# Performance work log

Measured on AMD Instinct MI355X. Metric: run time of the kernel, lower is better.

The kernel has to match this reference:

```python
import jax, jax.numpy as jnp
import numpy as np

N = 50000
E = 800000
IN_CH = 128
HID = 32
HEADS = 4
OUT_CH = 40
LEAKY = 0.2
BN_EPS = 1e-5


def _gat_layer(x, src, dst, W, a_src, a_dst, b, n_nodes, concat):
    # x: [N, F_in], W: [F_in, H*C], a_src/a_dst: [H, C], b: [H*C] or [C]
    H, C = a_src.shape
    h = (x @ W).reshape(n_nodes, H, C)                      # [N, H, C]
    e_s = jnp.einsum('nhc,hc->nh', h, a_src)                # [N, H]
    e_d = jnp.einsum('nhc,hc->nh', h, a_dst)                # [N, H]
    e = e_s[src] + e_d[dst]                                 # [E, H]
    e = jnp.where(e > 0, e, LEAKY * e)                      # LeakyReLU
    # segment softmax over incoming edges of each destination node
    m = jax.ops.segment_max(e, dst, num_segments=n_nodes)   # [N, H]
    ex = jnp.exp(e - m[dst])
    s = jax.ops.segment_sum(ex, dst, num_segments=n_nodes)  # [N, H]
    alpha = ex / s[dst]                                     # [E, H]
    out = jax.ops.segment_sum(h[src] * alpha[:, :, None], dst,
                              num_segments=n_nodes)         # [N, H, C]
    out = out.reshape(n_nodes, H * C) if concat else out.mean(axis=1)
    return out + b


def setup_inputs() -> dict:
    key = jax.random.key(0)
    ks = jax.random.split(key, 16)
    d1 = HEADS * HID  # 128
    inp = {
        'x': jax.random.normal(ks[0], (N, IN_CH), dtype=jnp.float32),
        'edge_index': jax.random.randint(ks[1], (2, E), 0, N, dtype=jnp.int64),
        # conv1 params (heads=4, concat)
        'W1': jax.random.normal(ks[2], (IN_CH, d1), dtype=jnp.float32) * 0.1,
        'a1_src': jax.random.normal(ks[3], (HEADS, HID), dtype=jnp.float32) * 0.1,
        'a1_dst': jax.random.normal(ks[4], (HEADS, HID), dtype=jnp.float32) * 0.1,
        'b1': jnp.zeros((d1,), dtype=jnp.float32),
        # BatchNorm1d(128) in eval mode
        'bn_gamma': jnp.ones((d1,), dtype=jnp.float32),
        'bn_beta': jnp.zeros((d1,), dtype=jnp.float32),
        'bn_mean': jax.random.normal(ks[5], (d1,), dtype=jnp.float32) * 0.1,
        'bn_var': jax.random.uniform(ks[6], (d1,), minval=0.5, maxval=1.5, dtype=jnp.float32),
        # conv2 params (heads=1, concat=False)
        'W2': jax.random.normal(ks[7], (d1, OUT_CH), dtype=jnp.float32) * 0.1,
        'a2_src': jax.random.normal(ks[8], (1, OUT_CH), dtype=jnp.float32) * 0.1,
        'a2_dst': jax.random.normal(ks[9], (1, OUT_CH), dtype=jnp.float32) * 0.1,
        'b2': jnp.zeros((OUT_CH,), dtype=jnp.float32),
    }
    return inp


def reference(x, edge_index, W1, a1_src, a1_dst, b1, bn_gamma, bn_beta,
              bn_mean, bn_var, W2, a2_src, a2_dst, b2):
    n = x.shape[0]
    loops = jnp.arange(n, dtype=edge_index.dtype)
    src = jnp.concatenate([edge_index[0], loops])  # PyG GATConv adds self-loops
    dst = jnp.concatenate([edge_index[1], loops])
    h = _gat_layer(x, src, dst, W1, a1_src, a1_dst, b1, n, concat=True)
    h = (h - bn_mean) / jnp.sqrt(bn_var + BN_EPS) * bn_gamma + bn_beta  # BN eval
    h = jax.nn.elu(h)
    # dropout is identity in eval mode
    out = _gat_layer(h, src, dst, W2, a2_src, a2_dst, b2, n, concat=False)
    return jax.nn.log_softmax(out, axis=1)
```

## Files before the change

kernel.cpp:

```cpp
#include <hip/hip_runtime.h>
#include <hip/hip_bf16.h>
#include <math.h>

#define NN 50000
#define NE 800000
#define ETOT (NE + NN)
#define LEAKY 0.2f
#define BN_EPS 1e-5f

#define NB 256
#define BSZ 196
#define NBB 128
#define EPB ((ETOT + NBB - 1) / NBB)

#define BN1 144
#define BN2 48

typedef unsigned short u16;
typedef unsigned int u32;
typedef short s16;
typedef __attribute__((ext_vector_type(8))) short bf16x8;
typedef __attribute__((ext_vector_type(4))) float f32x4;

__device__ __forceinline__ float bf2f(u32 u) {
    union { u32 i; float f; } x; x.i = u << 16; return x.f;
}
__device__ __forceinline__ u16 f2bf(float f) {
    __hip_bfloat16 b = __float2bfloat16(f);
    return *reinterpret_cast<u16*>(&b);
}


__global__ __launch_bounds__(256) void k_binA(const int* __restrict__ ei,
                                              int* __restrict__ cnt) {
    __shared__ int hist[NB];
    int t = threadIdx.x;
    for (int i = t; i < NB; i += 256) hist[i] = 0;
    __syncthreads();
    int e0 = blockIdx.x * EPB, e1 = min(e0 + EPB, ETOT);
    for (int e = e0 + t; e < e1; e += 256) {
        int dst = (e < NE) ? ei[NE + e] : (e - NE);
        atomicAdd(&hist[dst / BSZ], 1);
    }
    __syncthreads();
    for (int b = t; b < NB; b += 256) cnt[b * NBB + blockIdx.x] = hist[b];
}

__global__ __launch_bounds__(256) void k_scanA(const int* __restrict__ in,
                                               int* __restrict__ out,
                                               int* __restrict__ bsums, int n) {
    __shared__ int sh[256];
    int t = threadIdx.x;
    int i = blockIdx.x * 256 + t;
    int v = (i < n) ? in[i] : 0;
    sh[t] = v;
    __syncthreads();
    #pragma unroll
    for (int off = 1; off < 256; off <<= 1) {
        int u = (t >= off) ? sh[t - off] : 0;
        __syncthreads();
        sh[t] += u;
        __syncthreads();
    }
    if (i < n) out[i] = sh[t] - v;
    if (t == 255) bsums[blockIdx.x] = sh[t];
}

__global__ __launch_bounds__(256) void k_scanB(int* __restrict__ bsums, int nb) {
    __shared__ int sh[256];
    int t = threadIdx.x;
    int v = (t < nb) ? bsums[t] : 0;
    sh[t] = v;
    __syncthreads();
    #pragma unroll
    for (int off = 1; off < 256; off <<= 1) {
        int u = (t >= off) ? sh[t - off] : 0;
        __syncthreads();
        sh[t] += u;
        __syncthreads();
    }
    if (t < nb) bsums[t] = sh[t] - v;
}

__global__ void k_scanC(int* __restrict__ out, const int* __restrict__ bsums, int n) {
    int i = blockIdx.x * blockDim.x + threadIdx.x;
    if (i < n) out[i] += bsums[i >> 8];
}

__global__ __launch_bounds__(256) void k_binB(const int* __restrict__ ei,
                                              const int* __restrict__ excl,
                                              u32* __restrict__ packed) {
    __shared__ int cur[NB];
    int t = threadIdx.x;
    for (int b = t; b < NB; b += 256) cur[b] = excl[b * NBB + blockIdx.x];
    __syncthreads();
    int e0 = blockIdx.x * EPB, e1 = min(e0 + EPB, ETOT);
    for (int e = e0 + t; e < e1; e += 256) {
        int src, dst;
        if (e < NE) { src = ei[e]; dst = ei[NE + e]; }
        else        { src = e - NE; dst = e - NE; }
        int pos = atomicAdd(&cur[dst / BSZ], 1);
        packed[pos] = ((u32)src << 16) | (u32)dst;
    }
}

__global__ __launch_bounds__(256) void k_binC(const u32* __restrict__ packed,
                                              const int* __restrict__ excl,
                                              int* __restrict__ offsets,
                                              int* __restrict__ ssrc) {
    __shared__ int hist[256];
    __shared__ int sc[256];
    __shared__ int cur[256];
    int b = blockIdx.x, t = threadIdx.x;
    int n0 = b * BSZ;
    int base = excl[b * NBB];
    int next = (b < NB - 1) ? excl[(b + 1) * NBB] : ETOT;
    int total = next - base;
    hist[t] = 0;
    __syncthreads();
    for (int i = t; i < total; i += 256) {
        int dst = (int)(packed[base + i] & 0xffffu);
        atomicAdd(&hist[dst - n0], 1);
    }
    __syncthreads();
    int v = hist[t];
    sc[t] = v;
    __syncthreads();
    #pragma unroll
    for (int off = 1; off < 256; off <<= 1) {
        int u = (t >= off) ? sc[t - off] : 0;
        __syncthreads();
        sc[t] += u;
        __syncthreads();
    }
    int exl = sc[t] - v;
    int node = n0 + t;
    if (t <= BSZ && node <= NN) {
        if (t < BSZ || node == NN) offsets[node] = base + exl;
    }
    cur[t] = exl;
    __syncthreads();
    for (int i = t; i < total; i += 256) {
        u32 pv = packed[base + i];
        int dst = (int)(pv & 0xffffu);
        int pos = atomicAdd(&cur[dst - n0], 1);
        ssrc[base + pos] = (int)(pv >> 16);
    }
}

__global__ void k_prep(const float* __restrict__ W1, const float* __restrict__ a1s,
                       const float* __restrict__ a1d, const float* __restrict__ W2,
                       const float* __restrict__ a2s, const float* __restrict__ a2d,
                       u16* __restrict__ Wt1, u16* __restrict__ Wt2) {
    int tid = blockIdx.x * blockDim.x + threadIdx.x;
    int nth = gridDim.x * blockDim.x;
    for (int idx = tid; idx < BN1 * 128; idx += nth) {
        int n = idx >> 7, k = idx & 127;
        float v = 0.f;
        if (n < 128) v = W1[k * 128 + n];
        else if (n < 132) {
            int h = n - 128; float s = 0.f;
            for (int c = 0; c < 32; ++c) s += W1[k * 128 + h * 32 + c] * a1s[h * 32 + c];
            v = s;
        } else if (n < 136) {
            int h = n - 132; float s = 0.f;
            for (int c = 0; c < 32; ++c) s += W1[k * 128 + h * 32 + c] * a1d[h * 32 + c];
            v = s;
        }
        Wt1[idx] = f2bf(v);
    }
    for (int idx = tid; idx < BN2 * 128; idx += nth) {
        int n = idx >> 7, k = idx & 127;
        float v = 0.f;
        if (n < 40) v = W2[k * 40 + n];
        else if (n == 40) { float s = 0.f; for (int c = 0; c < 40; ++c) s += W2[k * 40 + c] * a2s[c]; v = s; }
        else if (n == 41) { float s = 0.f; for (int c = 0; c < 40; ++c) s += W2[k * 40 + c] * a2d[c]; v = s; }
        Wt2[idx] = f2bf(v);
    }
}

__global__ __launch_bounds__(256) void k_mm1(const float* __restrict__ x,
                                             const u16* __restrict__ Wt1,
                                             u16* __restrict__ h1b,
                                             float* __restrict__ es1,
                                             float* __restrict__ ed1) {
    __shared__ __align__(16) s16 As[128 * 128];
    __shared__ __align__(16) s16 Bs[BN1 * 128];
    int t = threadIdx.x;
    int row0 = blockIdx.x * 128;
    #pragma unroll
    for (int i = 0; i < 16; ++i) {
        int c = t + i * 256;
        int r = c >> 5, k0 = (c & 31) * 4;
        float4 v = make_float4(0.f, 0.f, 0.f, 0.f);
        int row = row0 + r;
        if (row < NN) v = *(const float4*)&x[(size_t)row * 128 + k0];
        u16 pk[4] = {f2bf(v.x), f2bf(v.y), f2bf(v.z), f2bf(v.w)};
        int byte = (r * 256 + k0 * 2) ^ ((r & 7) << 4);
        *(uint2*)((char*)As + byte) = *(uint2*)pk;
    }
    #pragma unroll
    for (int i = 0; i < 9; ++i) {
        int c = t + i * 256;
        int n = c >> 4, k0 = (c & 15) * 8;
        uint4 v = *(const uint4*)&Wt1[n * 128 + k0];
        int byte = (n * 256 + k0 * 2) ^ ((n & 7) << 4);
        *(uint4*)((char*)Bs + byte) = v;
    }
    __syncthreads();
    int wave = t >> 6, lane = t & 63;
    int lr = lane & 15, lq = lane >> 4;
    int wrow = wave * 32;
    f32x4 acc[2][9];
    #pragma unroll
    for (int a = 0; a < 2; ++a)
        #pragma unroll
        for (int b = 0; b < 9; ++b) acc[a][b] = (f32x4){0.f, 0.f, 0.f, 0.f};
    #pragma unroll
    for (int ks = 0; ks < 4; ++ks) {
        int kb = ks * 32 + lq * 8;
        bf16x8 af[2];
        #pragma unroll
        for (int rb = 0; rb < 2; ++rb) {
            int r = wrow + rb * 16 + lr;
            int byte = (r * 256 + kb * 2) ^ ((r & 7) << 4);
            af[rb] = *(bf16x8*)((char*)As + byte);
        }
        #pragma unroll
        for (int cb = 0; cb < 9; ++cb) {
            int n = cb * 16 + lr;
            int byte = (n * 256 + kb * 2) ^ ((n & 7) << 4);
            bf16x8 bfr = *(bf16x8*)((char*)Bs + byte);
            acc[0][cb] = __builtin_amdgcn_mfma_f32_16x16x32_bf16(af[0], bfr, acc[0][cb], 0, 0, 0);
            acc[1][cb] = __builtin_amdgcn_mfma_f32_16x16x32_bf16(af[1], bfr, acc[1][cb], 0, 0, 0);
        }
    }
    #pragma unroll
    for (int rb = 0; rb < 2; ++rb) {
        #pragma unroll
        for (int cb = 0; cb < 9; ++cb) {
            #pragma unroll
            for (int r = 0; r < 4; ++r) {
                int row = row0 + wrow + rb * 16 + lq * 4 + r;
                int col = cb * 16 + lr;
                if (row < NN) {
                    float v = acc[rb][cb][r];
                    if (col < 128) h1b[(size_t)row * 128 + col] = f2bf(v);
                    else if (col < 132) es1[row * 4 + (col - 128)] = v;
                    else if (col < 136) ed1[row * 4 + (col - 132)] = v;
                }
            }
        }
    }
}

__global__ __launch_bounds__(256) void k_mm2(const u16* __restrict__ hbnb,
                                             const u16* __restrict__ Wt2,
                                             float* __restrict__ h2,
                                             float* __restrict__ es2,
                                             float* __restrict__ ed2) {
    __shared__ __align__(16) s16 As[128 * 128];
    __shared__ __align__(16) s16 Bs[BN2 * 128];
    int t = threadIdx.x;
    int row0 = blockIdx.x * 128;
    #pragma unroll
    for (int i = 0; i < 8; ++i) {
        int c = t + i * 256;
        int r = c >> 4, k0 = (c & 15) * 8;
        uint4 v = make_uint4(0, 0, 0, 0);
        int row = row0 + r;
        if (row < NN) v = *(const uint4*)&hbnb[(size_t)row * 128 + k0];
        int byte = (r * 256 + k0 * 2) ^ ((r & 7) << 4);
        *(uint4*)((char*)As + byte) = v;
    }
    #pragma unroll
    for (int i = 0; i < 3; ++i) {
        int c = t + i * 256;
        int n = c >> 4, k0 = (c & 15) * 8;
        uint4 v = *(const uint4*)&Wt2[n * 128 + k0];
        int byte = (n * 256 + k0 * 2) ^ ((n & 7) << 4);
        *(uint4*)((char*)Bs + byte) = v;
    }
    __syncthreads();
    int wave = t >> 6, lane = t & 63;
    int lr = lane & 15, lq = lane >> 4;
    int wrow = wave * 32;
    f32x4 acc[2][3];
    #pragma unroll
    for (int a = 0; a < 2; ++a)
        #pragma unroll
        for (int b = 0; b < 3; ++b) acc[a][b] = (f32x4){0.f, 0.f, 0.f, 0.f};
    #pragma unroll
    for (int ks = 0; ks < 4; ++ks) {
        int kb = ks * 32 + lq * 8;
        bf16x8 af[2];
        #pragma unroll
        for (int rb = 0; rb < 2; ++rb) {
            int r = wrow + rb * 16 + lr;
            int byte = (r * 256 + kb * 2) ^ ((r & 7) << 4);
            af[rb] = *(bf16x8*)((char*)As + byte);
        }
        #pragma unroll
        for (int cb = 0; cb < 3; ++cb) {
            int n = cb * 16 + lr;
            int byte = (n * 256 + kb * 2) ^ ((n & 7) << 4);
            bf16x8 bfr = *(bf16x8*)((char*)Bs + byte);
            acc[0][cb] = __builtin_amdgcn_mfma_f32_16x16x32_bf16(af[0], bfr, acc[0][cb], 0, 0, 0);
            acc[1][cb] = __builtin_amdgcn_mfma_f32_16x16x32_bf16(af[1], bfr, acc[1][cb], 0, 0, 0);
        }
    }
    #pragma unroll
    for (int rb = 0; rb < 2; ++rb) {
        #pragma unroll
        for (int cb = 0; cb < 3; ++cb) {
            #pragma unroll
            for (int r = 0; r < 4; ++r) {
                int row = row0 + wrow + rb * 16 + lq * 4 + r;
                int col = cb * 16 + lr;
                if (row < NN) {
                    float v = acc[rb][cb][r];
                    if (col < 40) h2[(size_t)row * 40 + col] = v;
                    else if (col == 40) es2[row] = v;
                    else if (col == 41) ed2[row] = v;
                }
            }
        }
    }
}

__global__ __launch_bounds__(256) void k_agg1(
        const u16* __restrict__ h1b, const float* __restrict__ es,
        const float* __restrict__ ed, const int* __restrict__ offsets,
        const int* __restrict__ ssrc, const float* __restrict__ b1,
        const float* __restrict__ gamma, const float* __restrict__ beta,
        const float* __restrict__ mean, const float* __restrict__ var,
        u16* __restrict__ hbnb) {
    __shared__ float wlds[4][64][4];
    int wv = threadIdx.x >> 6;
    int node = blockIdx.x * 4 + wv;
    if (node >= NN) return;
    int l = threadIdx.x & 63;
    int head = l >> 4;
    int p0 = offsets[node], p1 = offsets[node + 1];
    float4 ed4 = *(const float4*)&ed[(size_t)node * 4];
    float4 sw4 = make_float4(0.f, 0.f, 0.f, 0.f);
    float acc0 = 0.f, acc1 = 0.f;
    const float* wp = &wlds[wv][0][head];
    for (int base = p0; base < p1; base += 64) {
        int cnt = min(64, p1 - base);
        int myidx = (l < cnt) ? ssrc[base + l] : 0;
        float4 w4 = make_float4(0.f, 0.f, 0.f, 0.f);
        if (l < cnt) {
            float4 e4 = *(const float4*)&es[(size_t)myidx * 4];
            float tv;
            tv = e4.x + ed4.x; tv = tv > 0.f ? tv : LEAKY * tv; w4.x = __expf(tv);
            tv = e4.y + ed4.y; tv = tv > 0.f ? tv : LEAKY * tv; w4.y = __expf(tv);
            tv = e4.z + ed4.z; tv = tv > 0.f ? tv : LEAKY * tv; w4.z = __expf(tv);
            tv = e4.w + ed4.w; tv = tv > 0.f ? tv : LEAKY * tv; w4.w = __expf(tv);
        }
        *(float4*)&wlds[wv][l][0] = w4;
        sw4.x += w4.x; sw4.y += w4.y; sw4.z += w4.z; sw4.w += w4.w;
        int j = 0;
        for (; j + 8 <= cnt; j += 8) {
            int s0 = __shfl(myidx, j);
            int s1 = __shfl(myidx, j + 1);
            int s2 = __shfl(myidx, j + 2);
            int s3 = __shfl(myidx, j + 3);
            int s4 = __shfl(myidx, j + 4);
            int s5 = __shfl(myidx, j + 5);
            int s6 = __shfl(myidx, j + 6);
            int s7 = __shfl(myidx, j + 7);
            u32 w0 = *(const u32*)&h1b[(size_t)s0 * 128 + 2 * l];
            u32 w1 = *(const u32*)&h1b[(size_t)s1 * 128 + 2 * l];
            u32 w2 = *(const u32*)&h1b[(size_t)s2 * 128 + 2 * l];
            u32 w3 = *(const u32*)&h1b[(size_t)s3 * 128 + 2 * l];
            u32 w4g = *(const u32*)&h1b[(size_t)s4 * 128 + 2 * l];
            u32 w5 = *(const u32*)&h1b[(size_t)s5 * 128 + 2 * l];
            u32 w6 = *(const u32*)&h1b[(size_t)s6 * 128 + 2 * l];
            u32 w7 = *(const u32*)&h1b[(size_t)s7 * 128 + 2 * l];
            float x0 = wp[(j + 0) * 4];
            float x1 = wp[(j + 1) * 4];
            float x2 = wp[(j + 2) * 4];
            float x3 = wp[(j + 3) * 4];
            float x4 = wp[(j + 4) * 4];
            float x5 = wp[(j + 5) * 4];
            float x6 = wp[(j + 6) * 4];
            float x7 = wp[(j + 7) * 4];
            acc0 = fmaf(x0, bf2f(w0 & 0xffffu), acc0);
            acc1 = fmaf(x0, bf2f(w0 >> 16), acc1);
            acc0 = fmaf(x1, bf2f(w1 & 0xffffu), acc0);
            acc1 = fmaf(x1, bf2f(w1 >> 16), acc1);
            acc0 = fmaf(x2, bf2f(w2 & 0xffffu), acc0);
            acc1 = fmaf(x2, bf2f(w2 >> 16), acc1);
            acc0 = fmaf(x3, bf2f(w3 & 0xffffu), acc0);
            acc1 = fmaf(x3, bf2f(w3 >> 16), acc1);
            acc0 = fmaf(x4, bf2f(w4g & 0xffffu), acc0);
            acc1 = fmaf(x4, bf2f(w4g >> 16), acc1);
            acc0 = fmaf(x5, bf2f(w5 & 0xffffu), acc0);
            acc1 = fmaf(x5, bf2f(w5 >> 16), acc1);
            acc0 = fmaf(x6, bf2f(w6 & 0xffffu), acc0);
            acc1 = fmaf(x6, bf2f(w6 >> 16), acc1);
            acc0 = fmaf(x7, bf2f(w7 & 0xffffu), acc0);
            acc1 = fmaf(x7, bf2f(w7 >> 16), acc1);
        }
        for (; j + 4 <= cnt; j += 4) {
            int s0 = __shfl(myidx, j);
            int s1 = __shfl(myidx, j + 1);
            int s2 = __shfl(myidx, j + 2);
            int s3 = __shfl(myidx, j + 3);
            u32 w0 = *(const u32*)&h1b[(size_t)s0 * 128 + 2 * l];
            u32 w1 = *(const u32*)&h1b[(size_t)s1 * 128 + 2 * l];
            u32 w2 = *(const u32*)&h1b[(size_t)s2 * 128 + 2 * l];
            u32 w3 = *(const u32*)&h1b[(size_t)s3 * 128 + 2 * l];
            float x0 = wp[(j + 0) * 4];
            float x1 = wp[(j + 1) * 4];
            float x2 = wp[(j + 2) * 4];
            float x3 = wp[(j + 3) * 4];
            acc0 = fmaf(x0, bf2f(w0 & 0xffffu), acc0);
            acc1 = fmaf(x0, bf2f(w0 >> 16), acc1);
            acc0 = fmaf(x1, bf2f(w1 & 0xffffu), acc0);
            acc1 = fmaf(x1, bf2f(w1 >> 16), acc1);
            acc0 = fmaf(x2, bf2f(w2 & 0xffffu), acc0);
            acc1 = fmaf(x2, bf2f(w2 >> 16), acc1);
            acc0 = fmaf(x3, bf2f(w3 & 0xffffu), acc0);
            acc1 = fmaf(x3, bf2f(w3 >> 16), acc1);
        }
        for (; j < cnt; ++j) {
            int s0 = __shfl(myidx, j);
            u32 w0 = *(const u32*)&h1b[(size_t)s0 * 128 + 2 * l];
            float x0 = wp[j * 4];
            acc0 = fmaf(x0, bf2f(w0 & 0xffffu), acc0);
            acc1 = fmaf(x0, bf2f(w0 >> 16), acc1);
        }
    }
    #pragma unroll
    for (int off = 1; off < 64; off <<= 1) {
        sw4.x += __shfl_xor(sw4.x, off);
        sw4.y += __shfl_xor(sw4.y, off);
        sw4.z += __shfl_xor(sw4.z, off);
        sw4.w += __shfl_xor(sw4.w, off);
    }
    float s = (head == 0) ? sw4.x : (head == 1) ? sw4.y : (head == 2) ? sw4.z : sw4.w;
    float inv = 1.f / s;
    int i0 = 2 * l, i1 = 2 * l + 1;
    float o0 = acc0 * inv + b1[i0];
    float o1 = acc1 * inv + b1[i1];
    o0 = (o0 - mean[i0]) * rsqrtf(var[i0] + BN_EPS) * gamma[i0] + beta[i0];
    o1 = (o1 - mean[i1]) * rsqrtf(var[i1] + BN_EPS) * gamma[i1] + beta[i1];
    o0 = o0 > 0.f ? o0 : __expf(o0) - 1.f;
    o1 = o1 > 0.f ? o1 : __expf(o1) - 1.f;
    u32 pk = (u32)f2bf(o0) | ((u32)f2bf(o1) << 16);
    *(u32*)&hbnb[(size_t)node * 128 + 2 * l] = pk;
}

__global__ __launch_bounds__(256) void k_agg2(
        const float* __restrict__ h2, const float* __restrict__ es,
        const float* __restrict__ ed, const int* __restrict__ offsets,
        const int* __restrict__ ssrc, const float* __restrict__ b2,
        float* __restrict__ out) {
    int node = blockIdx.x * 4 + (threadIdx.x >> 6);
    if (node >= NN) return;
    int l = threadIdx.x & 63;
    int lmod = (l < 40) ? l : (l - 40);
    int p0 = offsets[node], p1 = offsets[node + 1];
    float edv = ed[node];
    float swacc = 0.f, acc = 0.f;
    bool pay = (l < 40);
    for (int base = p0; base < p1; base += 64) {
        int cnt = min(64, p1 - base);
        int myidx = (l < cnt) ? ssrc[base + l] : 0;
        float mw = 0.f;
        if (l < cnt) {
            float e = es[myidx] + edv;
            e = e > 0.f ? e : LEAKY * e;
            mw = __expf(e);
        }
        swacc += mw;
        int j = 0;
        for (; j + 8 <= cnt; j += 8) {
            int s0 = __shfl(myidx, j);
            int s1 = __shfl(myidx, j + 1);
            int s2 = __shfl(myidx, j + 2);
            int s3 = __shfl(myidx, j + 3);
            int s4 = __shfl(myidx, j + 4);
            int s5 = __shfl(myidx, j + 5);
            int s6 = __shfl(myidx, j + 6);
            int s7 = __shfl(myidx, j + 7);
            float x0 = __shfl(mw, j);
            float x1 = __shfl(mw, j + 1);
            float x2 = __shfl(mw, j + 2);
            float x3 = __shfl(mw, j + 3);
            float x4 = __shfl(mw, j + 4);
            float x5 = __shfl(mw, j + 5);
            float x6 = __shfl(mw, j + 6);
            float x7 = __shfl(mw, j + 7);
            float h0 = h2[(size_t)s0 * 40 + lmod];
            float h1v = h2[(size_t)s1 * 40 + lmod];
            float h2v = h2[(size_t)s2 * 40 + lmod];
            float h3 = h2[(size_t)s3 * 40 + lmod];
            float h4 = h2[(size_t)s4 * 40 + lmod];
            float h5 = h2[(size_t)s5 * 40 + lmod];
            float h6 = h2[(size_t)s6 * 40 + lmod];
            float h7 = h2[(size_t)s7 * 40 + lmod];
            acc = fmaf(x0, h0, acc);
            acc = fmaf(x1, h1v, acc);
            acc = fmaf(x2, h2v, acc);
            acc = fmaf(x3, h3, acc);
            acc = fmaf(x4, h4, acc);
            acc = fmaf(x5, h5, acc);
            acc = fmaf(x6, h6, acc);
            acc = fmaf(x7, h7, acc);
        }
        for (; j + 4 <= cnt; j += 4) {
            int s0 = __shfl(myidx, j);
            int s1 = __shfl(myidx, j + 1);
            int s2 = __shfl(myidx, j + 2);
            int s3 = __shfl(myidx, j + 3);
            float x0 = __shfl(mw, j);
            float x1 = __shfl(mw, j + 1);
            float x2 = __shfl(mw, j + 2);
            float x3 = __shfl(mw, j + 3);
            float h0 = h2[(size_t)s0 * 40 + lmod];
            float h1v = h2[(size_t)s1 * 40 + lmod];
            float h2v = h2[(size_t)s2 * 40 + lmod];
            float h3 = h2[(size_t)s3 * 40 + lmod];
            acc = fmaf(x0, h0, acc);
            acc = fmaf(x1, h1v, acc);
            acc = fmaf(x2, h2v, acc);
            acc = fmaf(x3, h3, acc);
        }
        for (; j < cnt; ++j) {
            int s0 = __shfl(myidx, j);
            float x0 = __shfl(mw, j);
            float h0 = h2[(size_t)s0 * 40 + lmod];
            acc = fmaf(x0, h0, acc);
        }
    }
    float s = swacc;
    #pragma unroll
    for (int off = 1; off < 64; off <<= 1) s += __shfl_xor(s, off);
    float v = acc / s + (pay ? b2[l] : 0.f);
    float mv = pay ? v : -1e30f;
    #pragma unroll
    for (int off = 1; off < 64; off <<= 1) mv = fmaxf(mv, __shfl_xor(mv, off));
    float ex = pay ? __expf(v - mv) : 0.f;
    #pragma unroll
    for (int off = 1; off < 64; off <<= 1) ex += __shfl_xor(ex, off);
    if (pay) out[(size_t)node * 40 + l] = v - mv - __logf(ex);
}

extern "C" void kernel_launch(void* const* d_in, const int* in_sizes, int n_in,
                              void* d_out, int out_size, void* d_ws, size_t ws_size,
                              hipStream_t stream) {
    const float* x   = (const float*)d_in[0];
    const int*   ei  = (const int*)d_in[1];
    const float* W1  = (const float*)d_in[2];
    const float* a1s = (const float*)d_in[3];
    const float* a1d = (const float*)d_in[4];
    const float* b1  = (const float*)d_in[5];
    const float* bng = (const float*)d_in[6];
    const float* bnb = (const float*)d_in[7];
    const float* bnm = (const float*)d_in[8];
    const float* bnv = (const float*)d_in[9];
    const float* W2  = (const float*)d_in[10];
    const float* a2s = (const float*)d_in[11];
    const float* a2d = (const float*)d_in[12];
    const float* b2  = (const float*)d_in[13];
    float* out = (float*)d_out;

    char* ws = (char*)d_ws;
    size_t off = 0;
    auto alloc = [&](size_t bytes) -> void* {
        void* p = ws + off;
        off = (off + bytes + 255) & ~(size_t)255;
        return p;
    };
    int*   cntb     = (int*)alloc((size_t)NB * NBB * 4);
    int*   excl     = (int*)alloc((size_t)NB * NBB * 4);
    int*   bsums    = (int*)alloc((size_t)NBB * 4);
    int*   offsets  = (int*)alloc((size_t)(NN + 1) * 4);
    u32*   packed   = (u32*)alloc((size_t)ETOT * 4);
    int*   ssrc     = (int*)alloc((size_t)ETOT * 4);
    u16*   Wt1      = (u16*)alloc((size_t)BN1 * 128 * 2);
    u16*   Wt2      = (u16*)alloc((size_t)BN2 * 128 * 2);
    u16*   h1b      = (u16*)alloc((size_t)NN * 128 * 2);
    float* es1      = (float*)alloc((size_t)NN * 4 * 4);
    float* ed1      = (float*)alloc((size_t)NN * 4 * 4);
    u16*   hbnb     = (u16*)alloc((size_t)NN * 128 * 2);
    float* h2       = (float*)alloc((size_t)NN * 40 * 4);
    float* es2      = (float*)alloc((size_t)NN * 4);
    float* ed2      = (float*)alloc((size_t)NN * 4);

    const int nscan = NB * NBB;
    k_prep<<<80, 256, 0, stream>>>(W1, a1s, a1d, W2, a2s, a2d, Wt1, Wt2);
    k_binA<<<NBB, 256, 0, stream>>>(ei, cntb);
    k_scanA<<<nscan / 256, 256, 0, stream>>>(cntb, excl, bsums, nscan);
    k_scanB<<<1, 256, 0, stream>>>(bsums, NBB);
    k_scanC<<<nscan / 256, 256, 0, stream>>>(excl, bsums, nscan);
    k_binB<<<NBB, 256, 0, stream>>>(ei, excl, packed);
    k_binC<<<NB, 256, 0, stream>>>(packed, excl, offsets, ssrc);
    k_mm1<<<(NN + 127) / 128, 256, 0, stream>>>(x, Wt1, h1b, es1, ed1);
    k_agg1<<<(NN + 3) / 4, 256, 0, stream>>>(h1b, es1, ed1, offsets, ssrc,
                                             b1, bng, bnb, bnm, bnv, hbnb);
    k_mm2<<<(NN + 127) / 128, 256, 0, stream>>>(hbnb, Wt2, h2, es2, ed2);
    k_agg2<<<(NN + 3) / 4, 256, 0, stream>>>(h2, es2, ed2, offsets, ssrc, b2, out);
}
```

Before: 146.7 us.

## Gather layer-1 neighbor rows with 16-byte loads across four edge groups

The layer-1 aggregation now splits each wave into four 16-lane groups, each handling a different edge. Each lane loads 8 bf16 channels with one 16-byte load instead of a 4-byte load per edge per lane, and the four partial sums are merged with cross-lane shuffles at the end. The aim is to cut the number of gather load instructions and make each edge's 256-byte row a single wide access. In exchange it adds more accumulator registers, clamped or masked tail iterations, and a final reduction, and only a quarter of the lanes do the epilogue.

```diff
diff --git a/kernel.cpp b/kernel.cpp
--- a/kernel.cpp
+++ b/kernel.cpp
@@ -24,6 +24,12 @@
 
 __device__ __forceinline__ float bf2f(u32 u) {
     union { u32 i; float f; } x; x.i = u << 16; return x.f;
+}
+__device__ __forceinline__ float bf2f_lo(u32 u) {
+    union { u32 i; float f; } x; x.i = u << 16; return x.f;
+}
+__device__ __forceinline__ float bf2f_hi(u32 u) {
+    union { u32 i; float f; } x; x.i = u & 0xffff0000u; return x.f;
 }
 __device__ __forceinline__ u16 f2bf(float f) {
     __hip_bfloat16 b = __float2bfloat16(f);
@@ -340,12 +346,15 @@
     int node = blockIdx.x * 4 + wv;
     if (node >= NN) return;
     int l = threadIdx.x & 63;
-    int head = l >> 4;
+    int g = l >> 4;
+    int c16 = l & 15;
+    int h = c16 >> 2;
     int p0 = offsets[node], p1 = offsets[node + 1];
     float4 ed4 = *(const float4*)&ed[(size_t)node * 4];
     float4 sw4 = make_float4(0.f, 0.f, 0.f, 0.f);
-    float acc0 = 0.f, acc1 = 0.f;
-    const float* wp = &wlds[wv][0][head];
+    float acc[8];
+    #pragma unroll
+    for (int i = 0; i < 8; ++i) acc[i] = 0.f;
     for (int base = p0; base < p1; base += 64) {
         int cnt = min(64, p1 - base);
         int myidx = (l < cnt) ? ssrc[base + l] : 0;
@@ -360,78 +369,38 @@
         }
         *(float4*)&wlds[wv][l][0] = w4;
         sw4.x += w4.x; sw4.y += w4.y; sw4.z += w4.z; sw4.w += w4.w;
-        int j = 0;
-        for (; j + 8 <= cnt; j += 8) {
-            int s0 = __shfl(myidx, j);
-            int s1 = __shfl(myidx, j + 1);
-            int s2 = __shfl(myidx, j + 2);
-            int s3 = __shfl(myidx, j + 3);
-            int s4 = __shfl(myidx, j + 4);
-            int s5 = __shfl(myidx, j + 5);
-            int s6 = __shfl(myidx, j + 6);
-            int s7 = __shfl(myidx, j + 7);
-            u32 w0 = *(const u32*)&h1b[(size_t)s0 * 128 + 2 * l];
-            u32 w1 = *(const u32*)&h1b[(size_t)s1 * 128 + 2 * l];
-            u32 w2 = *(const u32*)&h1b[(size_t)s2 * 128 + 2 * l];
-            u32 w3 = *(const u32*)&h1b[(size_t)s3 * 128 + 2 * l];
-            u32 w4g = *(const u32*)&h1b[(size_t)s4 * 128 + 2 * l];
-            u32 w5 = *(const u32*)&h1b[(size_t)s5 * 128 + 2 * l];
-            u32 w6 = *(const u32*)&h1b[(size_t)s6 * 128 + 2 * l];
-            u32 w7 = *(const u32*)&h1b[(size_t)s7 * 128 + 2 * l];
-            float x0 = wp[(j + 0) * 4];
-            float x1 = wp[(j + 1) * 4];
-            float x2 = wp[(j + 2) * 4];
-            float x3 = wp[(j + 3) * 4];
-            float x4 = wp[(j + 4) * 4];
-            float x5 = wp[(j + 5) * 4];
-            float x6 = wp[(j + 6) * 4];
-            float x7 = wp[(j + 7) * 4];
-            acc0 = fmaf(x0, bf2f(w0 & 0xffffu), acc0);
-            acc1 = fmaf(x0, bf2f(w0 >> 16), acc1);
-            acc0 = fmaf(x1, bf2f(w1 & 0xffffu), acc0);
-            acc1 = fmaf(x1, bf2f(w1 >> 16), acc1);
-            acc0 = fmaf(x2, bf2f(w2 & 0xffffu), acc0);
-            acc1 = fmaf(x2, bf2f(w2 >> 16), acc1);
-            acc0 = fmaf(x3, bf2f(w3 & 0xffffu), acc0);
-            acc1 = fmaf(x3, bf2f(w3 >> 16), acc1);
-            acc0 = fmaf(x4, bf2f(w4g & 0xffffu), acc0);
-            acc1 = fmaf(x4, bf2f(w4g >> 16), acc1);
-            acc0 = fmaf(x5, bf2f(w5 & 0xffffu), acc0);
-            acc1 = fmaf(x5, bf2f(w5 >> 16), acc1);
-            acc0 = fmaf(x6, bf2f(w6 & 0xffffu), acc0);
-            acc1 = fmaf(x6, bf2f(w6 >> 16), acc1);
-            acc0 = fmaf(x7, bf2f(w7 & 0xffffu), acc0);
-            acc1 = fmaf(x7, bf2f(w7 >> 16), acc1);
-        }
-        for (; j + 4 <= cnt; j += 4) {
-            int s0 = __shfl(myidx, j);
-            int s1 = __shfl(myidx, j + 1);
-            int s2 = __shfl(myidx, j + 2);
-            int s3 = __shfl(myidx, j + 3);
-            u32 w0 = *(const u32*)&h1b[(size_t)s0 * 128 + 2 * l];
-            u32 w1 = *(const u32*)&h1b[(size_t)s1 * 128 + 2 * l];
-            u32 w2 = *(const u32*)&h1b[(size_t)s2 * 128 + 2 * l];
-            u32 w3 = *(const u32*)&h1b[(size_t)s3 * 128 + 2 * l];
-            float x0 = wp[(j + 0) * 4];
-            float x1 = wp[(j + 1) * 4];
-            float x2 = wp[(j + 2) * 4];
-            float x3 = wp[(j + 3) * 4];
-            acc0 = fmaf(x0, bf2f(w0 & 0xffffu), acc0);
-            acc1 = fmaf(x0, bf2f(w0 >> 16), acc1);
-            acc0 = fmaf(x1, bf2f(w1 & 0xffffu), acc0);
-            acc1 = fmaf(x1, bf2f(w1 >> 16), acc1);
-            acc0 = fmaf(x2, bf2f(w2 & 0xffffu), acc0);
-            acc1 = fmaf(x2, bf2f(w2 >> 16), acc1);
-            acc0 = fmaf(x3, bf2f(w3 & 0xffffu), acc0);
-            acc1 = fmaf(x3, bf2f(w3 >> 16), acc1);
-        }
-        for (; j < cnt; ++j) {
-            int s0 = __shfl(myidx, j);
-            u32 w0 = *(const u32*)&h1b[(size_t)s0 * 128 + 2 * l];
-            float x0 = wp[j * 4];
-            acc0 = fmaf(x0, bf2f(w0 & 0xffffu), acc0);
-            acc1 = fmaf(x0, bf2f(w0 >> 16), acc1);
-        }
+        __builtin_amdgcn_wave_barrier();
+        for (int j = 0; j < cnt; j += 8) {
+            int e0 = j + g, e1 = j + 4 + g;
+            int c0v = min(e0, cnt - 1), c1v = min(e1, cnt - 1);
+            int s0 = __shfl(myidx, c0v);
+            int s1 = __shfl(myidx, c1v);
+            float x0 = (e0 < cnt) ? wlds[wv][c0v][h] : 0.f;
+            float x1 = (e1 < cnt) ? wlds[wv][c1v][h] : 0.f;
+            uint4 r0 = *(const uint4*)&h1b[(size_t)s0 * 128 + c16 * 8];
+            uint4 r1 = *(const uint4*)&h1b[(size_t)s1 * 128 + c16 * 8];
+            acc[0] = fmaf(x0, bf2f_lo(r0.x), acc[0]);
+            acc[1] = fmaf(x0, bf2f_hi(r0.x), acc[1]);
+            acc[2] = fmaf(x0, bf2f_lo(r0.y), acc[2]);
+            acc[3] = fmaf(x0, bf2f_hi(r0.y), acc[3]);
+            acc[4] = fmaf(x0, bf2f_lo(r0.z), acc[4]);
+            acc[5] = fmaf(x0, bf2f_hi(r0.z), acc[5]);
+            acc[6] = fmaf(x0, bf2f_lo(r0.w), acc[6]);
+            acc[7] = fmaf(x0, bf2f_hi(r0.w), acc[7]);
+            acc[0] = fmaf(x1, bf2f_lo(r1.x), acc[0]);
+            acc[1] = fmaf(x1, bf2f_hi(r1.x), acc[1]);
+            acc[2] = fmaf(x1, bf2f_lo(r1.y), acc[2]);
+            acc[3] = fmaf(x1, bf2f_hi(r1.y), acc[3]);
+            acc[4] = fmaf(x1, bf2f_lo(r1.z), acc[4]);
+            acc[5] = fmaf(x1, bf2f_hi(r1.z), acc[5]);
+            acc[6] = fmaf(x1, bf2f_lo(r1.w), acc[6]);
+            acc[7] = fmaf(x1, bf2f_hi(r1.w), acc[7]);
+        }
+    }
+    #pragma unroll
+    for (int i = 0; i < 8; ++i) {
+        acc[i] += __shfl_xor(acc[i], 16);
+        acc[i] += __shfl_xor(acc[i], 32);
     }
     #pragma unroll
     for (int off = 1; off < 64; off <<= 1) {
@@ -440,17 +409,30 @@
         sw4.z += __shfl_xor(sw4.z, off);
         sw4.w += __shfl_xor(sw4.w, off);
     }
-    float s = (head == 0) ? sw4.x : (head == 1) ? sw4.y : (head == 2) ? sw4.z : sw4.w;
-    float inv = 1.f / s;
-    int i0 = 2 * l, i1 = 2 * l + 1;
-    float o0 = acc0 * inv + b1[i0];
-    float o1 = acc1 * inv + b1[i1];
-    o0 = (o0 - mean[i0]) * rsqrtf(var[i0] + BN_EPS) * gamma[i0] + beta[i0];
-    o1 = (o1 - mean[i1]) * rsqrtf(var[i1] + BN_EPS) * gamma[i1] + beta[i1];
-    o0 = o0 > 0.f ? o0 : __expf(o0) - 1.f;
-    o1 = o1 > 0.f ? o1 : __expf(o1) - 1.f;
-    u32 pk = (u32)f2bf(o0) | ((u32)f2bf(o1) << 16);
-    *(u32*)&hbnb[(size_t)node * 128 + 2 * l] = pk;
+    if (g == 0) {
+        float s = (h == 0) ? sw4.x : (h == 1) ? sw4.y : (h == 2) ? sw4.z : sw4.w;
+        float inv = 1.f / s;
+        int c0 = c16 * 8;
+        float4 b1a = *(const float4*)&b1[c0],    b1b = *(const float4*)&b1[c0 + 4];
+        float4 mna = *(const float4*)&mean[c0],  mnb = *(const float4*)&mean[c0 + 4];
+        float4 vra = *(const float4*)&var[c0],   vrb = *(const float4*)&var[c0 + 4];
+        float4 gma = *(const float4*)&gamma[c0], gmb = *(const float4*)&gamma[c0 + 4];
+        float4 bta = *(const float4*)&beta[c0],  btb = *(const float4*)&beta[c0 + 4];
+        float bv[8] = {b1a.x, b1a.y, b1a.z, b1a.w, b1b.x, b1b.y, b1b.z, b1b.w};
+        float mn[8] = {mna.x, mna.y, mna.z, mna.w, mnb.x, mnb.y, mnb.z, mnb.w};
+        float vr[8] = {vra.x, vra.y, vra.z, vra.w, vrb.x, vrb.y, vrb.z, vrb.w};
+        float gm[8] = {gma.x, gma.y, gma.z, gma.w, gmb.x, gmb.y, gmb.z, gmb.w};
+        float bt[8] = {bta.x, bta.y, bta.z, bta.w, btb.x, btb.y, btb.z, btb.w};
+        u16 pk[8];
+        #pragma unroll
+        for (int i = 0; i < 8; ++i) {
+            float o = acc[i] * inv + bv[i];
+            o = (o - mn[i]) * rsqrtf(vr[i] + BN_EPS) * gm[i] + bt[i];
+            o = o > 0.f ? o : __expf(o) - 1.f;
+            pk[i] = f2bf(o);
+        }
+        *(uint4*)&hbnb[(size_t)node * 128 + c0] = *(uint4*)pk;
+    }
 }
 
 __global__ __launch_bounds__(256) void k_agg2(
```

Result: no change. 147.6 us (+0.6%).
